# Kernel tuning notes

Measured on AMD Instinct MI355X. Metric: run time of the kernel, lower is better.

## Reference

```python
import jax, jax.numpy as jnp
import numpy as np

D_MODEL = 512
D_INNER = 1024   # expand * d_model
D_STATE = 16
D_CONV = 4
DT_RANK = 32     # ceil(d_model / 16)
N_LAYERS = 4
N_PRED_LAYERS = 2
FEAT = 128
LN_EPS = 1e-5


def _ln(x, w, b):
    m = x.mean(-1, keepdims=True)
    v = ((x - m) ** 2).mean(-1, keepdims=True)
    return (x - m) * jax.lax.rsqrt(v + LN_EPS) * w + b


def _silu(x):
    return x * jax.nn.sigmoid(x)


def _causal_conv(x, w, b):
    # depthwise causal conv1d: x (B,L,C), w (C,K), b (C,)
    K = w.shape[1]
    L = x.shape[1]
    xp = jnp.pad(x, ((0, 0), (K - 1, 0), (0, 0)))
    y = b
    for k in range(K):
        y = y + xp[:, k:k + L, :] * w[:, k]
    return y


def _mamba(x, in_w, conv_w, conv_b, xp_w, dt_w, dt_b, Alog, Dp, out_w):
    # x: (B,L,d_model)
    xz = jnp.einsum('bld,ed->ble', x, in_w)          # (B,L,2*d_inner)
    xi, z = jnp.split(xz, 2, axis=-1)
    xc = _silu(_causal_conv(xi, conv_w, conv_b))     # (B,L,d_inner)
    dbc = jnp.einsum('blc,ec->ble', xc, xp_w)        # (B,L,dt_rank+2N)
    dt = dbc[..., :DT_RANK]
    Bm = dbc[..., DT_RANK:DT_RANK + D_STATE]         # (B,L,N)
    Cm = dbc[..., DT_RANK + D_STATE:]                # (B,L,N)
    delta = jax.nn.softplus(jnp.einsum('blr,cr->blc', dt, dt_w) + dt_b)  # (B,L,d_inner)
    A = -jnp.exp(Alog)                               # (d_inner,N), negative
    dA = jnp.exp(delta[..., None] * A)               # (B,L,d_inner,N)
    dBu = delta[..., None] * Bm[:, :, None, :] * xc[..., None]

    def step(h, inp):
        dA_t, dBu_t, C_t = inp
        h = dA_t * h + dBu_t                         # (B,d_inner,N)
        y = jnp.einsum('bcn,bn->bc', h, C_t)
        return h, y

    h0 = jnp.zeros((x.shape[0], D_INNER, D_STATE), x.dtype)
    _, ys = jax.lax.scan(step, h0, (dA.transpose(1, 0, 2, 3),
                                    dBu.transpose(1, 0, 2, 3),
                                    Cm.transpose(1, 0, 2)))
    y = ys.transpose(1, 0, 2) + Dp * xc              # skip connection D*u
    y = y * _silu(z)
    return jnp.einsum('blc,dc->bld', y, out_w)


def _forward(x, inp_w, inp_b, enc_ln_w, enc_ln_b, enc_in_w, enc_conv_w, enc_conv_b,
             enc_xp_w, enc_dt_w, enc_dt_b, enc_Alog, enc_D, enc_out_w,
             fin_ln_w, fin_ln_b, prd_ln_w, prd_ln_b, prd_in_w, prd_conv_w, prd_conv_b,
             prd_xp_w, prd_dt_w, prd_dt_b, prd_Alog, prd_D, prd_out_w,
             prd_nrm_w, prd_nrm_b, prd_proj_w, prd_proj_b):
    # MambaEncoder: input_proj + n_layers pre-norm residual Mamba blocks + final LN
    h = jnp.einsum('blf,df->bld', x, inp_w) + inp_b
    for i in range(N_LAYERS):
        h = h + _mamba(_ln(h, enc_ln_w[i], enc_ln_b[i]),
                       enc_in_w[i], enc_conv_w[i], enc_conv_b[i], enc_xp_w[i],
                       enc_dt_w[i], enc_dt_b[i], enc_Alog[i], enc_D[i], enc_out_w[i])
    ctx = _ln(h, fin_ln_w, fin_ln_b)
    # MambaPredictor: small causal mamba stack + norm + proj
    p = ctx
    for i in range(N_PRED_LAYERS):
        p = p + _mamba(_ln(p, prd_ln_w[i], prd_ln_b[i]),
                       prd_in_w[i], prd_conv_w[i], prd_conv_b[i], prd_xp_w[i],
                       prd_dt_w[i], prd_dt_b[i], prd_Alog[i], prd_D[i], prd_out_w[i])
    p = _ln(p, prd_nrm_w, prd_nrm_b)
    preds = jnp.einsum('bld,ed->ble', p, prd_proj_w) + prd_proj_b
    return preds


def _mamba_params(key, n, scale=0.02):
    ks = jax.random.split(key, 6)
    arange_A = jnp.tile(jnp.log(jnp.arange(1, D_STATE + 1, dtype=jnp.float32)), (n, D_INNER, 1))
    return dict(
        in_w=jax.random.normal(ks[0], (n, 2 * D_INNER, D_MODEL)) * scale,
        conv_w=jax.random.normal(ks[1], (n, D_INNER, D_CONV)) * scale,
        conv_b=jnp.zeros((n, D_INNER)),
        xp_w=jax.random.normal(ks[2], (n, DT_RANK + 2 * D_STATE, D_INNER)) * scale,
        dt_w=jax.random.normal(ks[3], (n, D_INNER, DT_RANK)) * scale,
        dt_b=jnp.full((n, D_INNER), jnp.log(jnp.expm1(0.01))),  # inv-softplus(0.01)
        Alog=arange_A,
        D=jnp.ones((n, D_INNER)),
        out_w=jax.random.normal(ks[4], (n, D_MODEL, D_INNER)) * scale,
    )


def setup_inputs() -> dict:
    key = jax.random.key(0)
    ks = jax.random.split(key, 8)
    enc = _mamba_params(ks[0], N_LAYERS)
    prd = _mamba_params(ks[1], N_PRED_LAYERS)
    return {
        'x': jax.random.normal(ks[2], (2, 1024, FEAT), dtype=jnp.float32),
        'inp_w': jax.random.normal(ks[3], (D_MODEL, FEAT)) * 0.02,
        'inp_b': jnp.zeros((D_MODEL,)),
        'enc_ln_w': jnp.ones((N_LAYERS, D_MODEL)), 'enc_ln_b': jnp.zeros((N_LAYERS, D_MODEL)),
        'enc_in_w': enc['in_w'], 'enc_conv_w': enc['conv_w'], 'enc_conv_b': enc['conv_b'],
        'enc_xp_w': enc['xp_w'], 'enc_dt_w': enc['dt_w'], 'enc_dt_b': enc['dt_b'],
        'enc_Alog': enc['Alog'], 'enc_D': enc['D'], 'enc_out_w': enc['out_w'],
        'fin_ln_w': jnp.ones((D_MODEL,)), 'fin_ln_b': jnp.zeros((D_MODEL,)),
        'prd_ln_w': jnp.ones((N_PRED_LAYERS, D_MODEL)), 'prd_ln_b': jnp.zeros((N_PRED_LAYERS, D_MODEL)),
        'prd_in_w': prd['in_w'], 'prd_conv_w': prd['conv_w'], 'prd_conv_b': prd['conv_b'],
        'prd_xp_w': prd['xp_w'], 'prd_dt_w': prd['dt_w'], 'prd_dt_b': prd['dt_b'],
        'prd_Alog': prd['Alog'], 'prd_D': prd['D'], 'prd_out_w': prd['out_w'],
        'prd_nrm_w': jnp.ones((D_MODEL,)), 'prd_nrm_b': jnp.zeros((D_MODEL,)),
        'prd_proj_w': jax.random.normal(ks[4], (D_MODEL, D_MODEL)) * 0.02,
        'prd_proj_b': jnp.zeros((D_MODEL,)),
    }


def reference(x, inp_w, inp_b, enc_ln_w, enc_ln_b, enc_in_w, enc_conv_w, enc_conv_b,
              enc_xp_w, enc_dt_w, enc_dt_b, enc_Alog, enc_D, enc_out_w,
              fin_ln_w, fin_ln_b, prd_ln_w, prd_ln_b, prd_in_w, prd_conv_w, prd_conv_b,
              prd_xp_w, prd_dt_w, prd_dt_b, prd_Alog, prd_D, prd_out_w,
              prd_nrm_w, prd_nrm_b, prd_proj_w, prd_proj_b):
    return _forward(x, inp_w, inp_b, enc_ln_w, enc_ln_b, enc_in_w, enc_conv_w, enc_conv_b,
                    enc_xp_w, enc_dt_w, enc_dt_b, enc_Alog, enc_D, enc_out_w,
                    fin_ln_w, fin_ln_b, prd_ln_w, prd_ln_b, prd_in_w, prd_conv_w, prd_conv_b,
                    prd_xp_w, prd_dt_w, prd_dt_b, prd_Alog, prd_D, prd_out_w,
                    prd_nrm_w, prd_nrm_b, prd_proj_w, prd_proj_b)
```

## Files before the change

### kernel.cpp

```cpp
#include <hip/hip_runtime.h>
#include <hip/hip_bf16.h>

using bf16 = __hip_bfloat16;
typedef __attribute__((ext_vector_type(8))) short short8;
typedef __attribute__((ext_vector_type(4))) float f32x4;
typedef __attribute__((ext_vector_type(4))) unsigned int uint4v;

static constexpr int LB = 2;
static constexpr int LL = 1024;
static constexpr int DM = 512;
static constexpr int DI = 1024;
static constexpr int DSN = 16;
static constexpr int RK = 32;
static constexpr int MR_ROWS = LB * LL;

static constexpr int NCHUNK = 64;
static constexpr int CH = LL / NCHUNK;

struct ConvArgs {
    const float* src[9];
    bf16*        dst[9];
    int          n4[9];
};

__global__ __launch_bounds__(256) void convert_bf16_multi(ConvArgs a) {
    const int s = blockIdx.y;
    const float4* __restrict__ src = (const float4*)a.src[s];
    bf16* __restrict__ dst = a.dst[s];
    const int n4 = a.n4[s];
    for (int i = blockIdx.x * 256 + threadIdx.x; i < n4; i += gridDim.x * 256) {
        float4 v = src[i];
        bf16 t[4] = {__float2bfloat16(v.x), __float2bfloat16(v.y),
                     __float2bfloat16(v.z), __float2bfloat16(v.w)};
        *(uint2*)(dst + (size_t)i * 4) = *(uint2*)t;
    }
}

__device__ __forceinline__ void ln_store(float* outrow, int tid, float a, float b) {
    ((float2*)outrow)[tid] = make_float2(a, b);
}
__device__ __forceinline__ void ln_store(bf16* outrow, int tid, float a, float b) {
    __hip_bfloat162 h;
    h.x = __float2bfloat16(a);
    h.y = __float2bfloat16(b);
    ((__hip_bfloat162*)outrow)[tid] = h;
}

template <typename T>
__global__ __launch_bounds__(256) void ln_kernel(const float* __restrict__ x,
                                                 const float* __restrict__ w,
                                                 const float* __restrict__ b,
                                                 T* __restrict__ out) {
    const int row = blockIdx.x;
    const int tid = threadIdx.x;
    const int wid = tid >> 6, lane = tid & 63;
    __shared__ float red[8];

    const float2 v = ((const float2*)(x + (size_t)row * DM))[tid];
    float s = v.x + v.y;
#pragma unroll
    for (int m = 1; m < 64; m <<= 1) s += __shfl_xor(s, m);
    if (lane == 0) red[wid] = s;
    __syncthreads();
    const float mean = (red[0] + red[1] + red[2] + red[3]) * (1.f / DM);
    const float d0 = v.x - mean, d1 = v.y - mean;
    float s2 = d0 * d0 + d1 * d1;
#pragma unroll
    for (int m = 1; m < 64; m <<= 1) s2 += __shfl_xor(s2, m);
    if (lane == 0) red[4 + wid] = s2;
    __syncthreads();
    const float var = (red[4] + red[5] + red[6] + red[7]) * (1.f / DM);
    const float rs = rsqrtf(var + 1e-5f);
    const float2 wv = ((const float2*)w)[tid];
    const float2 bv = ((const float2*)b)[tid];
    ln_store(out + (size_t)row * DM, tid, d0 * rs * wv.x + bv.x, d1 * rs * wv.y + bv.y);
}

template <int BM, int BN, int BK, int EPI>
__global__ __launch_bounds__(256) void gemm_bt(const bf16* __restrict__ A, int lda,
                                               const bf16* __restrict__ B, int ldb,
                                               float* __restrict__ C, int ldc,
                                               int K, const float* __restrict__ bias) {
    static_assert(BK == 64, "swizzle assumes 128B LDS row stride");
    constexpr int MR = (BM / 2) / 16;
    constexpr int NR = (BN / 2) / 16;
    __shared__ __align__(16) bf16 sA[BM * BK];
    __shared__ __align__(16) bf16 sB[BN * BK];

    const int tid = threadIdx.x;
    const int lane = tid & 63, wid = tid >> 6;
    const int wr = wid >> 1, wc = wid & 1;
    const int m0 = blockIdx.y * BM, n0 = blockIdx.x * BN;
    const int kbase = (EPI == 2) ? blockIdx.z * K : 0;

    f32x4 acc[MR][NR] = {};

    constexpr int A_LD = BM * BK * 2 / (256 * 16);
    constexpr int B_LD = BN * BK * 2 / (256 * 16);
    static_assert(A_LD >= 1 && B_LD >= 1, "tile too small");

    for (int k0 = kbase; k0 < kbase + K; k0 += BK) {
#pragma unroll
        for (int i = 0; i < A_LD; ++i) {
            const int byte = (tid + i * 256) * 16;
            const int row = byte / (BK * 2), colb = byte % (BK * 2);
            const int sw = colb ^ ((row & 7) << 4);
            *(uint4v*)((char*)sA + row * (BK * 2) + sw) =
                *(const uint4v*)((const char*)A + ((size_t)(m0 + row) * lda + k0) * 2 + colb);
        }
#pragma unroll
        for (int i = 0; i < B_LD; ++i) {
            const int byte = (tid + i * 256) * 16;
            const int row = byte / (BK * 2), colb = byte % (BK * 2);
            const int sw = colb ^ ((row & 7) << 4);
            *(uint4v*)((char*)sB + row * (BK * 2) + sw) =
                *(const uint4v*)((const char*)B + ((size_t)(n0 + row) * ldb + k0) * 2 + colb);
        }
        __syncthreads();
#pragma unroll
        for (int kk = 0; kk < BK; kk += 32) {
            const int kb2 = (kk + (lane >> 4) * 8) * 2;
            short8 af[MR], bfr[NR];
#pragma unroll
            for (int m = 0; m < MR; ++m) {
                const int r = wr * (BM / 2) + m * 16 + (lane & 15);
                af[m] = *(const short8*)((const char*)sA + r * (BK * 2) + (kb2 ^ ((r & 7) << 4)));
            }
#pragma unroll
            for (int n = 0; n < NR; ++n) {
                const int r = wc * (BN / 2) + n * 16 + (lane & 15);
                bfr[n] = *(const short8*)((const char*)sB + r * (BK * 2) + (kb2 ^ ((r & 7) << 4)));
            }
#pragma unroll
            for (int m = 0; m < MR; ++m) {
#pragma unroll
                for (int n = 0; n < NR; ++n) {
                    acc[m][n] = __builtin_amdgcn_mfma_f32_16x16x32_bf16(af[m], bfr[n], acc[m][n], 0, 0, 0);
                }
            }
        }
        __syncthreads();
    }

#pragma unroll
    for (int m = 0; m < MR; ++m) {
#pragma unroll
        for (int n = 0; n < NR; ++n) {
            const int col = n0 + wc * (BN / 2) + n * 16 + (lane & 15);
            const float bv = (EPI == 1) ? bias[col] : 0.f;
#pragma unroll
            for (int j = 0; j < 4; ++j) {
                const int row = m0 + wr * (BM / 2) + m * 16 + (lane >> 4) * 4 + j;
                float v = acc[m][n][j] + bv;
                float* p = C + (size_t)row * ldc + col;
                if (EPI == 2) {
                    atomicAdd(p, v);
                } else {
                    if (EPI == 3) v += *p;
                    *p = v;
                }
            }
        }
    }
}

__global__ __launch_bounds__(256) void conv_silu_kernel(const float* __restrict__ xz,
                                                        const float* __restrict__ cw,
                                                        const float* __restrict__ cb,
                                                        float* __restrict__ xc,
                                                        bf16* __restrict__ xc_bf) {
    const int idx = blockIdx.x * 256 + threadIdx.x;
    const int c = idx & (DI - 1);
    const int r = idx >> 10;
    const int l = r & (LL - 1);
    const float* xi = xz + (size_t)r * (2 * DI) + c;
    const float4 w = *(const float4*)(cw + (size_t)c * 4);
    float acc = cb[c] + w.w * xi[0];
    if (l >= 1) acc += w.z * xi[-(2 * DI)];
    if (l >= 2) acc += w.y * xi[-(4 * DI)];
    if (l >= 3) acc += w.x * xi[-(6 * DI)];
    const float s = acc / (1.f + expf(-acc));
    xc[idx] = s;
    xc_bf[idx] = __float2bfloat16(s);
}

__global__ __launch_bounds__(256) void dtproj_kernel(const float* __restrict__ dbc,
                                                     const float* __restrict__ dtw,
                                                     const float* __restrict__ dtb,
                                                     float* __restrict__ delta) {
    __shared__ float sdt[RK];
    const int r = blockIdx.x;
    if (threadIdx.x < RK) sdt[threadIdx.x] = dbc[(size_t)r * 64 + threadIdx.x];
    __syncthreads();
    const int c = blockIdx.y * 256 + threadIdx.x;
    const float4* w4 = (const float4*)(dtw + (size_t)c * RK);
    float acc = dtb[c];
#pragma unroll
    for (int k = 0; k < RK / 4; ++k) {
        const float4 wv = w4[k];
        acc = fmaf(sdt[4 * k + 0], wv.x, acc);
        acc = fmaf(sdt[4 * k + 1], wv.y, acc);
        acc = fmaf(sdt[4 * k + 2], wv.z, acc);
        acc = fmaf(sdt[4 * k + 3], wv.w, acc);
    }
    delta[(size_t)r * DI + c] = (acc > 20.f) ? acc : log1pf(expf(acc));
}

__global__ __launch_bounds__(256) void scan_part1(const float* __restrict__ delta,
                                                  const float* __restrict__ xc,
                                                  const float* __restrict__ dbc,
                                                  const float* __restrict__ Alog,
                                                  float* __restrict__ psum,
                                                  float* __restrict__ ssum) {
    const int lane = threadIdx.x & 63;
    const int wsub = threadIdx.x >> 6;
    const int c = blockIdx.x * 64 + lane;
    const int chunk = blockIdx.y * 4 + wsub;
    const int b = blockIdx.z;
    const int r0 = b * LL + chunk * CH;

    float a2[DSN];
#pragma unroll
    for (int q = 0; q < 4; ++q) {
        const float4 al = *(const float4*)(Alog + (size_t)c * DSN + q * 4);
        a2[q * 4 + 0] = -expf(al.x) * 1.44269504f;
        a2[q * 4 + 1] = -expf(al.y) * 1.44269504f;
        a2[q * 4 + 2] = -expf(al.z) * 1.44269504f;
        a2[q * 4 + 3] = -expf(al.w) * 1.44269504f;
    }

    float h[DSN], P[DSN];
#pragma unroll
    for (int n = 0; n < DSN; ++n) { h[n] = 0.f; P[n] = 1.f; }

    for (int t = 0; t < CH; ++t) {
        const size_t r = r0 + t;
        const float d  = delta[r * DI + c];
        const float xv = xc[r * DI + c];
        const float dxv = d * xv;
        float Bv[DSN];
#pragma unroll
        for (int q = 0; q < 4; ++q)
            *(float4*)&Bv[q * 4] = *(const float4*)(dbc + r * 64 + 32 + q * 4);
#pragma unroll
        for (int n = 0; n < DSN; ++n) {
            const float dA = exp2f(d * a2[n]);
            h[n] = fmaf(dA, h[n], dxv * Bv[n]);
            P[n] *= dA;
        }
    }

    const size_t obase = ((size_t)(b * NCHUNK + chunk) * DSN) * DI + c;
#pragma unroll
    for (int n = 0; n < DSN; ++n) {
        psum[obase + (size_t)n * DI] = P[n];
        ssum[obase + (size_t)n * DI] = h[n];
    }
}

__global__ __launch_bounds__(256) void scan_combine(float* __restrict__ psum,
                                                    const float* __restrict__ ssum) {
    const int lane = threadIdx.x & 63;
    const int idx = blockIdx.y * 4 + (threadIdx.x >> 6);
    const int b = idx >> 4, n = idx & 15;
    const int c = blockIdx.x * 64 + lane;
    const size_t base = ((size_t)(b * NCHUNK) * DSN + n) * DI + c;
    const size_t stride = (size_t)DSN * DI;

    float h = 0.f;
    for (int j0 = 0; j0 < NCHUNK; j0 += 8) {
        float Pv[8], Sv[8];
#pragma unroll
        for (int u = 0; u < 8; ++u) {
            Pv[u] = psum[base + (j0 + u) * stride];
            Sv[u] = ssum[base + (j0 + u) * stride];
        }
#pragma unroll
        for (int u = 0; u < 8; ++u) {
            psum[base + (j0 + u) * stride] = h;
            h = fmaf(Pv[u], h, Sv[u]);
        }
    }
}

__global__ __launch_bounds__(256) void scan_part3(const float* __restrict__ delta,
                                                  const float* __restrict__ xc,
                                                  const float* __restrict__ xz,
                                                  const float* __restrict__ dbc,
                                                  const float* __restrict__ Alog,
                                                  const float* __restrict__ Dp,
                                                  const float* __restrict__ hin,
                                                  bf16* __restrict__ yg) {
    const int lane = threadIdx.x & 63;
    const int wsub = threadIdx.x >> 6;
    const int c = blockIdx.x * 64 + lane;
    const int chunk = blockIdx.y * 4 + wsub;
    const int b = blockIdx.z;
    const int r0 = b * LL + chunk * CH;

    float a2[DSN];
#pragma unroll
    for (int q = 0; q < 4; ++q) {
        const float4 al = *(const float4*)(Alog + (size_t)c * DSN + q * 4);
        a2[q * 4 + 0] = -expf(al.x) * 1.44269504f;
        a2[q * 4 + 1] = -expf(al.y) * 1.44269504f;
        a2[q * 4 + 2] = -expf(al.z) * 1.44269504f;
        a2[q * 4 + 3] = -expf(al.w) * 1.44269504f;
    }
    const float dp = Dp[c];

    float h[DSN];
    const size_t hbase = ((size_t)(b * NCHUNK + chunk) * DSN) * DI + c;
#pragma unroll
    for (int n = 0; n < DSN; ++n) h[n] = hin[hbase + (size_t)n * DI];

    for (int t = 0; t < CH; ++t) {
        const size_t r = r0 + t;
        const float d  = delta[r * DI + c];
        const float xv = xc[r * DI + c];
        const float zv = xz[r * (2 * DI) + DI + c];
        const float dxv = d * xv;
        float Bv[DSN], Cv[DSN];
#pragma unroll
        for (int q = 0; q < 4; ++q) {
            *(float4*)&Bv[q * 4] = *(const float4*)(dbc + r * 64 + 32 + q * 4);
            *(float4*)&Cv[q * 4] = *(const float4*)(dbc + r * 64 + 48 + q * 4);
        }
        float y0 = 0.f, y1 = 0.f, y2 = 0.f, y3 = 0.f;
#pragma unroll
        for (int q = 0; q < 4; ++q) {
            {
                const float dA = exp2f(d * a2[q * 4 + 0]);
                h[q * 4 + 0] = fmaf(dA, h[q * 4 + 0], dxv * Bv[q * 4 + 0]);
                y0 = fmaf(h[q * 4 + 0], Cv[q * 4 + 0], y0);
            }
            {
                const float dA = exp2f(d * a2[q * 4 + 1]);
                h[q * 4 + 1] = fmaf(dA, h[q * 4 + 1], dxv * Bv[q * 4 + 1]);
                y1 = fmaf(h[q * 4 + 1], Cv[q * 4 + 1], y1);
            }
            {
                const float dA = exp2f(d * a2[q * 4 + 2]);
                h[q * 4 + 2] = fmaf(dA, h[q * 4 + 2], dxv * Bv[q * 4 + 2]);
                y2 = fmaf(h[q * 4 + 2], Cv[q * 4 + 2], y2);
            }
            {
                const float dA = exp2f(d * a2[q * 4 + 3]);
                h[q * 4 + 3] = fmaf(dA, h[q * 4 + 3], dxv * Bv[q * 4 + 3]);
                y3 = fmaf(h[q * 4 + 3], Cv[q * 4 + 3], y3);
            }
        }
        const float y = (y0 + y1) + (y2 + y3);
        const float zs = zv / (1.f + expf(-zv));
        yg[r * DI + c] = __float2bfloat16((y + dp * xv) * zs);
    }
}

static void run_mamba_layer(hipStream_t stream, float* resid,
                            const float* ln_w, const float* ln_b,
                            const bf16* inw_bf,
                            const float* conv_w, const float* conv_b,
                            const bf16* xpw_bf,
                            const float* dt_w, const float* dt_b,
                            const float* Alog, const float* Dp,
                            const bf16* outw_bf,
                            bf16* ln_bf, float* xz, float* xc, bf16* xc_bf,
                            float* dbc, float* delta,
                            float* psum, float* ssum, bf16* yg_bf) {
    ln_kernel<bf16><<<MR_ROWS, 256, 0, stream>>>(resid, ln_w, ln_b, ln_bf);
    gemm_bt<64, 64, 64, 0><<<dim3(2 * DI / 64, MR_ROWS / 64), 256, 0, stream>>>(
        ln_bf, DM, inw_bf, DM, xz, 2 * DI, DM, nullptr);
    conv_silu_kernel<<<MR_ROWS * DI / 256, 256, 0, stream>>>(xz, conv_w, conv_b, xc, xc_bf);
    hipMemsetAsync(dbc, 0, (size_t)MR_ROWS * 64 * 4, stream);
    gemm_bt<32, 64, 64, 2><<<dim3(1, MR_ROWS / 32, 4), 256, 0, stream>>>(
        xc_bf, DI, xpw_bf, DI, dbc, 64, DI / 4, nullptr);
    dtproj_kernel<<<dim3(MR_ROWS, DI / 256), 256, 0, stream>>>(dbc, dt_w, dt_b, delta);
    scan_part1<<<dim3(DI / 64, NCHUNK / 4, LB), 256, 0, stream>>>(
        delta, xc, dbc, Alog, psum, ssum);
    scan_combine<<<dim3(DI / 64, (LB * DSN) / 4), 256, 0, stream>>>(psum, ssum);
    scan_part3<<<dim3(DI / 64, NCHUNK / 4, LB), 256, 0, stream>>>(
        delta, xc, xz, dbc, Alog, Dp, psum, yg_bf);
    gemm_bt<32, 64, 64, 3><<<dim3(DM / 64, MR_ROWS / 32), 256, 0, stream>>>(
        yg_bf, DI, outw_bf, DI, resid, DM, DI, nullptr);
}

extern "C" void kernel_launch(void* const* d_in, const int* in_sizes, int n_in,
                              void* d_out, int out_size, void* d_ws, size_t ws_size,
                              hipStream_t stream) {
    const float* x         = (const float*)d_in[0];
    const float* inp_w     = (const float*)d_in[1];
    const float* inp_b     = (const float*)d_in[2];
    const float* enc_ln_w  = (const float*)d_in[3];
    const float* enc_ln_b  = (const float*)d_in[4];
    const float* enc_in_w  = (const float*)d_in[5];
    const float* enc_conv_w= (const float*)d_in[6];
    const float* enc_conv_b= (const float*)d_in[7];
    const float* enc_xp_w  = (const float*)d_in[8];
    const float* enc_dt_w  = (const float*)d_in[9];
    const float* enc_dt_b  = (const float*)d_in[10];
    const float* enc_Alog  = (const float*)d_in[11];
    const float* enc_D     = (const float*)d_in[12];
    const float* enc_out_w = (const float*)d_in[13];
    const float* fin_ln_w  = (const float*)d_in[14];
    const float* fin_ln_b  = (const float*)d_in[15];
    const float* prd_ln_w  = (const float*)d_in[16];
    const float* prd_ln_b  = (const float*)d_in[17];
    const float* prd_in_w  = (const float*)d_in[18];
    const float* prd_conv_w= (const float*)d_in[19];
    const float* prd_conv_b= (const float*)d_in[20];
    const float* prd_xp_w  = (const float*)d_in[21];
    const float* prd_dt_w  = (const float*)d_in[22];
    const float* prd_dt_b  = (const float*)d_in[23];
    const float* prd_Alog  = (const float*)d_in[24];
    const float* prd_D     = (const float*)d_in[25];
    const float* prd_out_w = (const float*)d_in[26];
    const float* prd_nrm_w = (const float*)d_in[27];
    const float* prd_nrm_b = (const float*)d_in[28];
    const float* prd_proj_w= (const float*)d_in[29];
    const float* prd_proj_b= (const float*)d_in[30];

    char* wp = (char*)d_ws;
    auto carve = [&](size_t elems, size_t esz) {
        void* p = (void*)wp;
        wp += (elems * esz + 255) & ~(size_t)255;
        return p;
    };
    bf16* x_bf     = (bf16*)carve((size_t)MR_ROWS * 128, 2);
    bf16* inpw_bf  = (bf16*)carve((size_t)DM * 128, 2);
    bf16* einw_bf  = (bf16*)carve(4ull * 2 * DI * DM, 2);
    bf16* expw_bf  = (bf16*)carve(4ull * 64 * DI, 2);
    bf16* eoutw_bf = (bf16*)carve(4ull * DM * DI, 2);
    bf16* pinw_bf  = (bf16*)carve(2ull * 2 * DI * DM, 2);
    bf16* pxpw_bf  = (bf16*)carve(2ull * 64 * DI, 2);
    bf16* poutw_bf = (bf16*)carve(2ull * DM * DI, 2);
    bf16* projw_bf = (bf16*)carve((size_t)DM * DM, 2);
    float* hbuf    = (float*)carve((size_t)MR_ROWS * DM, 4);
    float* pbuf    = (float*)carve((size_t)MR_ROWS * DM, 4);
    bf16* ln_bf    = (bf16*)carve((size_t)MR_ROWS * DM, 2);
    float* xz      = (float*)carve((size_t)MR_ROWS * 2 * DI, 4);
    float* xc      = (float*)carve((size_t)MR_ROWS * DI, 4);
    bf16* xc_bf    = (bf16*)carve((size_t)MR_ROWS * DI, 2);
    float* dbc     = (float*)carve((size_t)MR_ROWS * 64, 4);
    float* delta   = (float*)carve((size_t)MR_ROWS * DI, 4);
    float* psum    = (float*)carve((size_t)LB * NCHUNK * DSN * DI, 4);
    float* ssum    = (float*)carve((size_t)LB * NCHUNK * DSN * DI, 4);
    bf16* yg_bf    = (bf16*)carve((size_t)MR_ROWS * DI, 2);

    ConvArgs ca;
    const float* csrc[9] = {x, inp_w, enc_in_w, enc_xp_w, enc_out_w,
                            prd_in_w, prd_xp_w, prd_out_w, prd_proj_w};
    bf16* cdst[9] = {x_bf, inpw_bf, einw_bf, expw_bf, eoutw_bf,
                     pinw_bf, pxpw_bf, poutw_bf, projw_bf};
    const int cn[9] = {MR_ROWS * 128, DM * 128, 4 * 2 * DI * DM, 4 * 64 * DI, 4 * DM * DI,
                       2 * 2 * DI * DM, 2 * 64 * DI, 2 * DM * DI, DM * DM};
    for (int i = 0; i < 9; ++i) { ca.src[i] = csrc[i]; ca.dst[i] = cdst[i]; ca.n4[i] = cn[i] / 4; }
    convert_bf16_multi<<<dim3(128, 9), 256, 0, stream>>>(ca);

    gemm_bt<32, 64, 64, 1><<<dim3(DM / 64, MR_ROWS / 32), 256, 0, stream>>>(
        x_bf, 128, inpw_bf, 128, hbuf, DM, 128, inp_b);

    for (int i = 0; i < 4; ++i) {
        run_mamba_layer(stream, hbuf,
                        enc_ln_w + (size_t)i * DM, enc_ln_b + (size_t)i * DM,
                        einw_bf + (size_t)i * 2 * DI * DM,
                        enc_conv_w + (size_t)i * DI * 4, enc_conv_b + (size_t)i * DI,
                        expw_bf + (size_t)i * 64 * DI,
                        enc_dt_w + (size_t)i * DI * RK, enc_dt_b + (size_t)i * DI,
                        enc_Alog + (size_t)i * DI * DSN, enc_D + (size_t)i * DI,
                        eoutw_bf + (size_t)i * DM * DI,
                        ln_bf, xz, xc, xc_bf, dbc, delta, psum, ssum, yg_bf);
    }

    ln_kernel<float><<<MR_ROWS, 256, 0, stream>>>(hbuf, fin_ln_w, fin_ln_b, pbuf);

    for (int i = 0; i < 2; ++i) {
        run_mamba_layer(stream, pbuf,
                        prd_ln_w + (size_t)i * DM, prd_ln_b + (size_t)i * DM,
                        pinw_bf + (size_t)i * 2 * DI * DM,
                        prd_conv_w + (size_t)i * DI * 4, prd_conv_b + (size_t)i * DI,
                        pxpw_bf + (size_t)i * 64 * DI,
                        prd_dt_w + (size_t)i * DI * RK, prd_dt_b + (size_t)i * DI,
                        prd_Alog + (size_t)i * DI * DSN, prd_D + (size_t)i * DI,
                        poutw_bf + (size_t)i * DM * DI,
                        ln_bf, xz, xc, xc_bf, dbc, delta, psum, ssum, yg_bf);
    }

    ln_kernel<bf16><<<MR_ROWS, 256, 0, stream>>>(pbuf, prd_nrm_w, prd_nrm_b, ln_bf);
    gemm_bt<32, 64, 64, 1><<<dim3(DM / 64, MR_ROWS / 32), 256, 0, stream>>>(
        ln_bf, DM, projw_bf, DM, (float*)d_out, DM, DM, prd_proj_b);

    (void)in_sizes; (void)n_in; (void)out_size; (void)ws_size;
}
```

Before: 755.6 us.

## Fuse dt projection into scan, stage GEMM tiles via direct global-to-LDS loads

Removes the separate dtproj kernel by computing delta (dt projection plus softplus) inside scan_part1, using a dt weight matrix transposed once per call so loads are coalesced per channel. The memset of dbc is folded into the conv_silu kernel. The GEMM tile staging switches from register round-trips to global_load_lds 16-byte loads with a per-wave XOR swizzle. This cuts kernel launches and delta round-trips, but adds 32 weight registers per scan thread and redundant dbc reads per channel.

```diff
diff --git a/kernel.cpp b/kernel.cpp
--- a/kernel.cpp
+++ b/kernel.cpp
@@ -4,7 +4,6 @@
 using bf16 = __hip_bfloat16;
 typedef __attribute__((ext_vector_type(8))) short short8;
 typedef __attribute__((ext_vector_type(4))) float f32x4;
-typedef __attribute__((ext_vector_type(4))) unsigned int uint4v;
 
 static constexpr int LB = 2;
 static constexpr int LL = 1024;
@@ -16,6 +15,12 @@
 
 static constexpr int NCHUNK = 64;
 static constexpr int CH = LL / NCHUNK;
+
+__device__ __forceinline__ void gload16(const void* g, void* l) {
+    __builtin_amdgcn_global_load_lds(
+        (__attribute__((address_space(1))) void*)(g),
+        (__attribute__((address_space(3))) void*)(l), 16, 0, 0);
+}
 
 struct ConvArgs {
     const float* src[9];
@@ -36,6 +41,18 @@
     }
 }
 
+__global__ __launch_bounds__(256) void transpose_dtw(const float* __restrict__ enc_dtw,
+                                                     const float* __restrict__ prd_dtw,
+                                                     float* __restrict__ out) {
+    const int layer = blockIdx.y;
+    const float* src = (layer < 4) ? enc_dtw + (size_t)layer * DI * RK
+                                   : prd_dtw + (size_t)(layer - 4) * DI * RK;
+    float* dst = out + (size_t)layer * RK * DI;
+    const int idx = blockIdx.x * 256 + threadIdx.x;
+    const int k = idx >> 10, c = idx & (DI - 1);
+    dst[idx] = src[(size_t)c * RK + k];
+}
+
 __device__ __forceinline__ void ln_store(float* outrow, int tid, float a, float b) {
     ((float2*)outrow)[tid] = make_float2(a, b);
 }
@@ -81,11 +98,12 @@
                                                const bf16* __restrict__ B, int ldb,
                                                float* __restrict__ C, int ldc,
                                                int K, const float* __restrict__ bias) {
-    static_assert(BK == 64, "swizzle assumes 128B LDS row stride");
+    static_assert(BK == 64, "layout assumes 128B LDS row");
+    static_assert(BM % 32 == 0 && BN % 32 == 0, "wave staging granularity");
     constexpr int MR = (BM / 2) / 16;
     constexpr int NR = (BN / 2) / 16;
-    __shared__ __align__(16) bf16 sA[BM * BK];
-    __shared__ __align__(16) bf16 sB[BN * BK];
+    __shared__ __align__(16) char sA[BM * 128];
+    __shared__ __align__(16) char sB[BN * 128];
 
     const int tid = threadIdx.x;
     const int lane = tid & 63, wid = tid >> 6;
@@ -95,27 +113,23 @@
 
     f32x4 acc[MR][NR] = {};
 
-    constexpr int A_LD = BM * BK * 2 / (256 * 16);
-    constexpr int B_LD = BN * BK * 2 / (256 * 16);
-    static_assert(A_LD >= 1 && B_LD >= 1, "tile too small");
-
-    for (int k0 = kbase; k0 < kbase + K; k0 += BK) {
-#pragma unroll
-        for (int i = 0; i < A_LD; ++i) {
-            const int byte = (tid + i * 256) * 16;
-            const int row = byte / (BK * 2), colb = byte % (BK * 2);
-            const int sw = colb ^ ((row & 7) << 4);
-            *(uint4v*)((char*)sA + row * (BK * 2) + sw) =
-                *(const uint4v*)((const char*)A + ((size_t)(m0 + row) * lda + k0) * 2 + colb);
-        }
-#pragma unroll
-        for (int i = 0; i < B_LD; ++i) {
-            const int byte = (tid + i * 256) * 16;
-            const int row = byte / (BK * 2), colb = byte % (BK * 2);
-            const int sw = colb ^ ((row & 7) << 4);
-            *(uint4v*)((char*)sB + row * (BK * 2) + sw) =
-                *(const uint4v*)((const char*)B + ((size_t)(n0 + row) * ldb + k0) * 2 + colb);
-        }
+    const int lrow = lane >> 3;
+    const int lcol = (lane & 7) ^ lrow;
+    const size_t lda2 = (size_t)lda * 2, ldb2 = (size_t)ldb * 2;
+    const char* Ab = (const char*)A + (size_t)(m0 + wid * (BM / 4) + lrow) * lda2
+                     + lcol * 16 + (size_t)kbase * 2;
+    const char* Bb = (const char*)B + (size_t)(n0 + wid * (BN / 4) + lrow) * ldb2
+                     + lcol * 16 + (size_t)kbase * 2;
+    char* sAw = sA + wid * (BM / 4) * 128;
+    char* sBw = sB + wid * (BN / 4) * 128;
+
+    for (int k0 = 0; k0 < K; k0 += BK) {
+#pragma unroll
+        for (int i = 0; i < BM / 32; ++i)
+            gload16(Ab + (size_t)i * 8 * lda2 + (size_t)k0 * 2, sAw + i * 1024);
+#pragma unroll
+        for (int i = 0; i < BN / 32; ++i)
+            gload16(Bb + (size_t)i * 8 * ldb2 + (size_t)k0 * 2, sBw + i * 1024);
         __syncthreads();
 #pragma unroll
         for (int kk = 0; kk < BK; kk += 32) {
@@ -124,12 +138,12 @@
 #pragma unroll
             for (int m = 0; m < MR; ++m) {
                 const int r = wr * (BM / 2) + m * 16 + (lane & 15);
-                af[m] = *(const short8*)((const char*)sA + r * (BK * 2) + (kb2 ^ ((r & 7) << 4)));
+                af[m] = *(const short8*)(sA + r * 128 + (kb2 ^ ((r & 7) << 4)));
             }
 #pragma unroll
             for (int n = 0; n < NR; ++n) {
                 const int r = wc * (BN / 2) + n * 16 + (lane & 15);
-                bfr[n] = *(const short8*)((const char*)sB + r * (BK * 2) + (kb2 ^ ((r & 7) << 4)));
+                bfr[n] = *(const short8*)(sB + r * 128 + (kb2 ^ ((r & 7) << 4)));
             }
 #pragma unroll
             for (int m = 0; m < MR; ++m) {
@@ -168,7 +182,11 @@
                                                         const float* __restrict__ cw,
                                                         const float* __restrict__ cb,
                                                         float* __restrict__ xc,
-                                                        bf16* __restrict__ xc_bf) {
+                                                        bf16* __restrict__ xc_bf,
+                                                        float* __restrict__ dbc_zero) {
+    if (blockIdx.x < 128) {
+        ((float4*)dbc_zero)[blockIdx.x * 256 + threadIdx.x] = make_float4(0.f, 0.f, 0.f, 0.f);
+    }
     const int idx = blockIdx.x * 256 + threadIdx.x;
     const int c = idx & (DI - 1);
     const int r = idx >> 10;
@@ -184,32 +202,12 @@
     xc_bf[idx] = __float2bfloat16(s);
 }
 
-__global__ __launch_bounds__(256) void dtproj_kernel(const float* __restrict__ dbc,
-                                                     const float* __restrict__ dtw,
-                                                     const float* __restrict__ dtb,
-                                                     float* __restrict__ delta) {
-    __shared__ float sdt[RK];
-    const int r = blockIdx.x;
-    if (threadIdx.x < RK) sdt[threadIdx.x] = dbc[(size_t)r * 64 + threadIdx.x];
-    __syncthreads();
-    const int c = blockIdx.y * 256 + threadIdx.x;
-    const float4* w4 = (const float4*)(dtw + (size_t)c * RK);
-    float acc = dtb[c];
-#pragma unroll
-    for (int k = 0; k < RK / 4; ++k) {
-        const float4 wv = w4[k];
-        acc = fmaf(sdt[4 * k + 0], wv.x, acc);
-        acc = fmaf(sdt[4 * k + 1], wv.y, acc);
-        acc = fmaf(sdt[4 * k + 2], wv.z, acc);
-        acc = fmaf(sdt[4 * k + 3], wv.w, acc);
-    }
-    delta[(size_t)r * DI + c] = (acc > 20.f) ? acc : log1pf(expf(acc));
-}
-
-__global__ __launch_bounds__(256) void scan_part1(const float* __restrict__ delta,
-                                                  const float* __restrict__ xc,
+__global__ __launch_bounds__(256) void scan_part1(const float* __restrict__ xc,
                                                   const float* __restrict__ dbc,
                                                   const float* __restrict__ Alog,
+                                                  const float* __restrict__ dtw_t,
+                                                  const float* __restrict__ dtb,
+                                                  float* __restrict__ delta,
                                                   float* __restrict__ psum,
                                                   float* __restrict__ ssum) {
     const int lane = threadIdx.x & 63;
@@ -219,6 +217,11 @@
     const int b = blockIdx.z;
     const int r0 = b * LL + chunk * CH;
 
+    float wv[RK];
+#pragma unroll
+    for (int k = 0; k < RK; ++k) wv[k] = dtw_t[(size_t)k * DI + c];
+    const float bdt = dtb[c];
+
     float a2[DSN];
 #pragma unroll
     for (int q = 0; q < 4; ++q) {
@@ -235,7 +238,18 @@
 
     for (int t = 0; t < CH; ++t) {
         const size_t r = r0 + t;
-        const float d  = delta[r * DI + c];
+        float acc = bdt;
+#pragma unroll
+        for (int q = 0; q < RK / 4; ++q) {
+            const float4 d4 = *(const float4*)(dbc + r * 64 + q * 4);
+            acc = fmaf(d4.x, wv[q * 4 + 0], acc);
+            acc = fmaf(d4.y, wv[q * 4 + 1], acc);
+            acc = fmaf(d4.z, wv[q * 4 + 2], acc);
+            acc = fmaf(d4.w, wv[q * 4 + 3], acc);
+        }
+        const float d = (acc > 20.f) ? acc : log1pf(expf(acc));
+        delta[r * DI + c] = d;
+
         const float xv = xc[r * DI + c];
         const float dxv = d * xv;
         float Bv[DSN];
@@ -361,7 +375,7 @@
                             const bf16* inw_bf,
                             const float* conv_w, const float* conv_b,
                             const bf16* xpw_bf,
-                            const float* dt_w, const float* dt_b,
+                            const float* dtw_t, const float* dt_b,
                             const float* Alog, const float* Dp,
                             const bf16* outw_bf,
                             bf16* ln_bf, float* xz, float* xc, bf16* xc_bf,
@@ -370,13 +384,11 @@
     ln_kernel<bf16><<<MR_ROWS, 256, 0, stream>>>(resid, ln_w, ln_b, ln_bf);
     gemm_bt<64, 64, 64, 0><<<dim3(2 * DI / 64, MR_ROWS / 64), 256, 0, stream>>>(
         ln_bf, DM, inw_bf, DM, xz, 2 * DI, DM, nullptr);
-    conv_silu_kernel<<<MR_ROWS * DI / 256, 256, 0, stream>>>(xz, conv_w, conv_b, xc, xc_bf);
-    hipMemsetAsync(dbc, 0, (size_t)MR_ROWS * 64 * 4, stream);
+    conv_silu_kernel<<<MR_ROWS * DI / 256, 256, 0, stream>>>(xz, conv_w, conv_b, xc, xc_bf, dbc);
     gemm_bt<32, 64, 64, 2><<<dim3(1, MR_ROWS / 32, 4), 256, 0, stream>>>(
         xc_bf, DI, xpw_bf, DI, dbc, 64, DI / 4, nullptr);
-    dtproj_kernel<<<dim3(MR_ROWS, DI / 256), 256, 0, stream>>>(dbc, dt_w, dt_b, delta);
     scan_part1<<<dim3(DI / 64, NCHUNK / 4, LB), 256, 0, stream>>>(
-        delta, xc, dbc, Alog, psum, ssum);
+        xc, dbc, Alog, dtw_t, dt_b, delta, psum, ssum);
     scan_combine<<<dim3(DI / 64, (LB * DSN) / 4), 256, 0, stream>>>(psum, ssum);
     scan_part3<<<dim3(DI / 64, NCHUNK / 4, LB), 256, 0, stream>>>(
         delta, xc, xz, dbc, Alog, Dp, psum, yg_bf);
@@ -434,6 +446,7 @@
     bf16* pxpw_bf  = (bf16*)carve(2ull * 64 * DI, 2);
     bf16* poutw_bf = (bf16*)carve(2ull * DM * DI, 2);
     bf16* projw_bf = (bf16*)carve((size_t)DM * DM, 2);
+    float* dtwt    = (float*)carve(6ull * RK * DI, 4);
     float* hbuf    = (float*)carve((size_t)MR_ROWS * DM, 4);
     float* pbuf    = (float*)carve((size_t)MR_ROWS * DM, 4);
     bf16* ln_bf    = (bf16*)carve((size_t)MR_ROWS * DM, 2);
@@ -455,6 +468,7 @@
                        2 * 2 * DI * DM, 2 * 64 * DI, 2 * DM * DI, DM * DM};
     for (int i = 0; i < 9; ++i) { ca.src[i] = csrc[i]; ca.dst[i] = cdst[i]; ca.n4[i] = cn[i] / 4; }
     convert_bf16_multi<<<dim3(128, 9), 256, 0, stream>>>(ca);
+    transpose_dtw<<<dim3(RK * DI / 256, 6), 256, 0, stream>>>(enc_dt_w, prd_dt_w, dtwt);
 
     gemm_bt<32, 64, 64, 1><<<dim3(DM / 64, MR_ROWS / 32), 256, 0, stream>>>(
         x_bf, 128, inpw_bf, 128, hbuf, DM, 128, inp_b);
@@ -465,7 +479,7 @@
                         einw_bf + (size_t)i * 2 * DI * DM,
                         enc_conv_w + (size_t)i * DI * 4, enc_conv_b + (size_t)i * DI,
                         expw_bf + (size_t)i * 64 * DI,
-                        enc_dt_w + (size_t)i * DI * RK, enc_dt_b + (size_t)i * DI,
+                        dtwt + (size_t)i * RK * DI, enc_dt_b + (size_t)i * DI,
                         enc_Alog + (size_t)i * DI * DSN, enc_D + (size_t)i * DI,
                         eoutw_bf + (size_t)i * DM * DI,
                         ln_bf, xz, xc, xc_bf, dbc, delta, psum, ssum, yg_bf);
@@ -479,7 +493,7 @@
                         pinw_bf + (size_t)i * 2 * DI * DM,
                         prd_conv_w + (size_t)i * DI * 4, prd_conv_b + (size_t)i * DI,
                         pxpw_bf + (size_t)i * 64 * DI,
-                        prd_dt_w + (size_t)i * DI * RK, prd_dt_b + (size_t)i * DI,
+                        dtwt + (size_t)(4 + i) * RK * DI, prd_dt_b + (size_t)i * DI,
                         prd_Alog + (size_t)i * DI * DSN, prd_D + (size_t)i * DI,
                         poutw_bf + (size_t)i * DM * DI,
                         ln_bf, xz, xc, xc_bf, dbc, delta, psum, ssum, yg_bf);
```

New measurement: 652.3 us. -13.7%, faster.
